# Performance work log

Measured on AMD Instinct MI355X. Metric: run time of the kernel, lower is better.

Reference implementation:

```python
import jax, jax.numpy as jnp
import numpy as np

N = 40000      # nodes
E = 20000      # hyperedges
M = 640000     # incidences
D = 128        # num_features == num_classes == MLP_hidden
ALPHA = 0.1
EPS = 1e-5


def _layernorm(h, g, b):
    mu = jnp.mean(h, axis=-1, keepdims=True)
    var = jnp.mean((h - mu) ** 2, axis=-1, keepdims=True)
    return (h - mu) * jax.lax.rsqrt(var + EPS) * g + b


def _mlp(x, w1, b1, g, be, w2, b2):
    h = x @ w1 + b1
    h = jax.nn.relu(_layernorm(h, g, be))
    return h @ w2 + b2


def _scatter_mean(vals, idx, num_segments):
    s = jax.ops.segment_sum(vals, idx, num_segments=num_segments)
    cnt = jax.ops.segment_sum(jnp.ones((vals.shape[0],), vals.dtype), idx,
                              num_segments=num_segments)
    return s / jnp.maximum(cnt, 1.0)[:, None]


def setup_inputs() -> dict:
    key = jax.random.key(0)
    ks = jax.random.split(key, 16)
    x = jax.random.normal(ks[0], (N, D), dtype=jnp.float32)
    vertex = jax.random.randint(ks[1], (M,), 0, N)
    edges = jax.random.randint(ks[2], (M,), 0, E)
    edge_index = jnp.stack([vertex, edges]).astype(jnp.int64)

    def lin(k, fin, fout):
        s = 1.0 / np.sqrt(fin)
        kw, kb = jax.random.split(k)
        return (jax.random.uniform(kw, (fin, fout), jnp.float32, -s, s),
                jax.random.uniform(kb, (fout,), jnp.float32, -s, s))

    w1_1, b1_1 = lin(ks[3], D, D)
    w1_2, b1_2 = lin(ks[4], D, D)
    w2_1, b2_1 = lin(ks[5], 2 * D, D)
    w2_2, b2_2 = lin(ks[6], D, D)
    g1 = jnp.ones((D,), jnp.float32)
    be1 = jnp.zeros((D,), jnp.float32)
    g2 = jnp.ones((D,), jnp.float32)
    be2 = jnp.zeros((D,), jnp.float32)
    return {"x": x, "w1_1": w1_1, "b1_1": b1_1, "g1": g1, "be1": be1,
            "w1_2": w1_2, "b1_2": b1_2, "w2_1": w2_1, "b2_1": b2_1,
            "g2": g2, "be2": be2, "w2_2": w2_2, "b2_2": b2_2,
            "edge_index": edge_index}


def reference(x, w1_1, b1_1, g1, be1, w1_2, b1_2,
              w2_1, b2_1, g2, be2, w2_2, b2_2, edge_index):
    vertex = edge_index[0]
    edges = edge_index[1]
    X0 = x
    # gather -> MLP1 -> scatter-mean onto hyperedges
    Xve = _mlp(x[vertex], w1_1, b1_1, g1, be1, w1_2, b1_2)   # [M, D]
    Xe = _scatter_mean(Xve, edges, E)                         # [E, D]
    # gather back -> concat -> MLP2 -> scatter-mean onto nodes
    Xev = Xe[edges]                                           # [M, D]
    Xev = _mlp(jnp.concatenate([x[vertex], Xev], axis=-1),
               w2_1, b2_1, g2, be2, w2_2, b2_2)               # [M, D]
    Xv = _scatter_mean(Xev, vertex, N)                        # [N, D]
    return (1.0 - ALPHA) * Xv + ALPHA * X0
```

## Files before the change

kernel.cpp:

```cpp
#include <hip/hip_runtime.h>

#define DF 128
constexpr int NN = 40000;
constexpr int EE = 20000;
constexpr int MM = 640000;
constexpr float EPSF = 1e-5f;
constexpr float ALPHA = 0.1f;
constexpr int SE = 88;
constexpr int SV = 56;

__global__ __launch_bounds__(256) void buildk(const int* __restrict__ ei,
                                              int* __restrict__ cnt_e,
                                              int* __restrict__ cnt_v,
                                              ushort* __restrict__ lst_e,
                                              ushort* __restrict__ lst_v) {
  int m = blockIdx.x * 256 + threadIdx.x;
  int v = ei[m];
  int e = ei[MM + m];
  int pe = atomicAdd(&cnt_e[e], 1);
  lst_e[e * SE + pe] = (ushort)v;
  int pv = atomicAdd(&cnt_v[v], 1);
  lst_v[v * SV + pv] = (ushort)e;
}

__global__ __launch_bounds__(128) void combok(const float* __restrict__ w1_2,
                                              const float* __restrict__ b1_2,
                                              const float* __restrict__ w2_1,
                                              float* __restrict__ Wc,
                                              float* __restrict__ bc) {
  const float* w2b = w2_1 + 128 * DF;
  int j = threadIdx.x;
  if (blockIdx.x < 128) {
    int i = blockIdx.x;
    float s = 0.0f;
    for (int k = 0; k < 128; ++k) s += w1_2[i * DF + k] * w2b[k * DF + j];
    Wc[i * DF + j] = s;
  } else {
    float s = 0.0f;
    for (int k = 0; k < 128; ++k) s += b1_2[k] * w2b[k * DF + j];
    bc[j] = s;
  }
}

__global__ __launch_bounds__(256) void gather1(const float* __restrict__ H1,
                                               const int* __restrict__ cnt_e,
                                               const ushort* __restrict__ lst_e,
                                               float* __restrict__ Hemean) {
  int e = blockIdx.x * 4 + (threadIdx.x >> 6);
  int lane = threadIdx.x & 63;
  int g = lane >> 4;
  int l = lane & 15;
  int deg = cnt_e[e];
  const ushort* lst = lst_e + e * SE;
  float4 acc0 = make_float4(0.f, 0.f, 0.f, 0.f);
  float4 acc1 = make_float4(0.f, 0.f, 0.f, 0.f);
  for (int i = g; i < deg; i += 4) {
    int v = lst[i];
    const float* src = H1 + (size_t)v * DF + l * 8;
    float4 h0 = *reinterpret_cast<const float4*>(src);
    float4 h1 = *reinterpret_cast<const float4*>(src + 4);
    acc0.x += h0.x; acc0.y += h0.y; acc0.z += h0.z; acc0.w += h0.w;
    acc1.x += h1.x; acc1.y += h1.y; acc1.z += h1.z; acc1.w += h1.w;
  }
  #pragma unroll
  for (int mask = 16; mask <= 32; mask <<= 1) {
    acc0.x += __shfl_xor(acc0.x, mask); acc0.y += __shfl_xor(acc0.y, mask);
    acc0.z += __shfl_xor(acc0.z, mask); acc0.w += __shfl_xor(acc0.w, mask);
    acc1.x += __shfl_xor(acc1.x, mask); acc1.y += __shfl_xor(acc1.y, mask);
    acc1.z += __shfl_xor(acc1.z, mask); acc1.w += __shfl_xor(acc1.w, mask);
  }
  if (g == 0) {
    float sc = 1.0f / (float)(deg > 1 ? deg : 1);
    float* dst = Hemean + (size_t)e * DF + l * 8;
    *reinterpret_cast<float4*>(dst) =
        make_float4(acc0.x * sc, acc0.y * sc, acc0.z * sc, acc0.w * sc);
    *reinterpret_cast<float4*>(dst + 4) =
        make_float4(acc1.x * sc, acc1.y * sc, acc1.z * sc, acc1.w * sc);
  }
}

__global__ __launch_bounds__(256) void gather2(const float* __restrict__ A2,
                                               const float* __restrict__ B,
                                               const float* __restrict__ sA,
                                               const float* __restrict__ qA,
                                               const float* __restrict__ sB,
                                               const float* __restrict__ qB,
                                               const int* __restrict__ cnt_v,
                                               const ushort* __restrict__ lst_v,
                                               const float* __restrict__ g2,
                                               const float* __restrict__ be2,
                                               float* __restrict__ Svmean) {
  int v = blockIdx.x * 4 + (threadIdx.x >> 6);
  int lane = threadIdx.x & 63;
  int g = lane >> 4;
  int l = lane & 15;
  const float* ap = A2 + (size_t)v * DF + l * 8;
  float4 a0 = *reinterpret_cast<const float4*>(ap);
  float4 a1 = *reinterpret_cast<const float4*>(ap + 4);
  float4 gv0 = *reinterpret_cast<const float4*>(g2 + l * 8);
  float4 gv1 = *reinterpret_cast<const float4*>(g2 + l * 8 + 4);
  float4 bv0 = *reinterpret_cast<const float4*>(be2 + l * 8);
  float4 bv1 = *reinterpret_cast<const float4*>(be2 + l * 8 + 4);
  float sAv = sA[v];
  float qAv = qA[v];
  int deg = cnt_v[v];
  const ushort* lst = lst_v + v * SV;
  float4 acc0 = make_float4(0.f, 0.f, 0.f, 0.f);
  float4 acc1 = make_float4(0.f, 0.f, 0.f, 0.f);
  for (int i = g; i < deg; i += 4) {
    int e = lst[i];
    const float* bp = B + (size_t)e * DF + l * 8;
    float4 b0 = *reinterpret_cast<const float4*>(bp);
    float4 b1 = *reinterpret_cast<const float4*>(bp + 4);
    float d = a0.x * b0.x + a0.y * b0.y + a0.z * b0.z + a0.w * b0.w +
              a1.x * b1.x + a1.y * b1.y + a1.z * b1.z + a1.w * b1.w;
    d += __shfl_xor(d, 1, 16);
    d += __shfl_xor(d, 2, 16);
    d += __shfl_xor(d, 4, 16);
    d += __shfl_xor(d, 8, 16);
    float s = sAv + sB[e];
    float q = qAv + qB[e] + 2.0f * d;
    float mean = s * (1.0f / 128.0f);
    float var = q * (1.0f / 128.0f) - mean * mean;
    float rs = rsqrtf(var + EPSF);
    float mrs = mean * rs;
    float t;
    t = (a0.x + b0.x) * rs - mrs; acc0.x += fmaxf(t * gv0.x + bv0.x, 0.f);
    t = (a0.y + b0.y) * rs - mrs; acc0.y += fmaxf(t * gv0.y + bv0.y, 0.f);
    t = (a0.z + b0.z) * rs - mrs; acc0.z += fmaxf(t * gv0.z + bv0.z, 0.f);
    t = (a0.w + b0.w) * rs - mrs; acc0.w += fmaxf(t * gv0.w + bv0.w, 0.f);
    t = (a1.x + b1.x) * rs - mrs; acc1.x += fmaxf(t * gv1.x + bv1.x, 0.f);
    t = (a1.y + b1.y) * rs - mrs; acc1.y += fmaxf(t * gv1.y + bv1.y, 0.f);
    t = (a1.z + b1.z) * rs - mrs; acc1.z += fmaxf(t * gv1.z + bv1.z, 0.f);
    t = (a1.w + b1.w) * rs - mrs; acc1.w += fmaxf(t * gv1.w + bv1.w, 0.f);
  }
  #pragma unroll
  for (int mask = 16; mask <= 32; mask <<= 1) {
    acc0.x += __shfl_xor(acc0.x, mask); acc0.y += __shfl_xor(acc0.y, mask);
    acc0.z += __shfl_xor(acc0.z, mask); acc0.w += __shfl_xor(acc0.w, mask);
    acc1.x += __shfl_xor(acc1.x, mask); acc1.y += __shfl_xor(acc1.y, mask);
    acc1.z += __shfl_xor(acc1.z, mask); acc1.w += __shfl_xor(acc1.w, mask);
  }
  if (g == 0) {
    float sc = 1.0f / (float)(deg > 1 ? deg : 1);
    float* dst = Svmean + (size_t)v * DF + l * 8;
    *reinterpret_cast<float4*>(dst) =
        make_float4(acc0.x * sc, acc0.y * sc, acc0.z * sc, acc0.w * sc);
    *reinterpret_cast<float4*>(dst + 4) =
        make_float4(acc1.x * sc, acc1.y * sc, acc1.z * sc, acc1.w * sc);
  }
}

template <int EPI, bool STATS>
__global__ __launch_bounds__(256) void gemm128(const float* __restrict__ A, int nrows,
                                               const float* __restrict__ W,
                                               const float* __restrict__ bias,
                                               const float* __restrict__ bias2,
                                               const int* __restrict__ cnt,
                                               const float* __restrict__ g,
                                               const float* __restrict__ be,
                                               const float* __restrict__ xres,
                                               float* __restrict__ C,
                                               float* __restrict__ sOut,
                                               float* __restrict__ qOut) {
  __shared__ float as[64 * 132];
  int tid = threadIdx.x;
  int rbase = blockIdx.x * 64;

  #pragma unroll
  for (int j = 0; j < 8; ++j) {
    int q = tid + j * 256;
    int row = q >> 5;
    int c4 = q & 31;
    int grow = rbase + row;
    float4 v = make_float4(0.f, 0.f, 0.f, 0.f);
    if (grow < nrows) {
      v = *reinterpret_cast<const float4*>(A + (size_t)grow * DF + c4 * 4);
    }
    *reinterpret_cast<float4*>(&as[row * 132 + c4 * 4]) = v;
  }
  __syncthreads();

  int tc = tid & 15;
  int tr = tid >> 4;
  int cbase = tc * 8;

  float acc[4][8];
  #pragma unroll
  for (int i = 0; i < 4; ++i)
    #pragma unroll
    for (int c = 0; c < 8; ++c) acc[i][c] = 0.0f;

  #pragma unroll 4
  for (int k = 0; k < 128; ++k) {
    float w[8];
    *reinterpret_cast<float4*>(&w[0]) = *reinterpret_cast<const float4*>(W + k * DF + cbase);
    *reinterpret_cast<float4*>(&w[4]) = *reinterpret_cast<const float4*>(W + k * DF + cbase + 4);
    float a[4];
    #pragma unroll
    for (int i = 0; i < 4; ++i) a[i] = as[(tr * 4 + i) * 132 + k];
    #pragma unroll
    for (int i = 0; i < 4; ++i)
      #pragma unroll
      for (int c = 0; c < 8; ++c) acc[i][c] += a[i] * w[c];
  }

  float bv[8];
  #pragma unroll
  for (int c = 0; c < 8; ++c) bv[c] = 0.0f;
  if (bias) {
    #pragma unroll
    for (int c = 0; c < 8; ++c) bv[c] = bias[cbase + c];
  }
  if (bias2) {
    #pragma unroll
    for (int c = 0; c < 8; ++c) bv[c] += bias2[cbase + c];
  }
  #pragma unroll
  for (int i = 0; i < 4; ++i)
    #pragma unroll
    for (int c = 0; c < 8; ++c) acc[i][c] += bv[c];

  if (STATS) {
    #pragma unroll
    for (int i = 0; i < 4; ++i) {
      float s = 0.f, q = 0.f;
      #pragma unroll
      for (int c = 0; c < 8; ++c) { s += acc[i][c]; q += acc[i][c] * acc[i][c]; }
      #pragma unroll
      for (int mask = 1; mask <= 8; mask <<= 1) {
        s += __shfl_xor(s, mask, 16);
        q += __shfl_xor(q, mask, 16);
      }
      if (tc == 0) {
        int grow = rbase + tr * 4 + i;
        if (grow < nrows) { sOut[grow] = s; qOut[grow] = q; }
      }
    }
  }

  if (EPI == 1) {
    float gv[8], bev[8];
    #pragma unroll
    for (int c = 0; c < 8; ++c) { gv[c] = g[cbase + c]; bev[c] = be[cbase + c]; }
    #pragma unroll
    for (int i = 0; i < 4; ++i) {
      float s = 0.f, s2 = 0.f;
      #pragma unroll
      for (int c = 0; c < 8; ++c) { s += acc[i][c]; s2 += acc[i][c] * acc[i][c]; }
      #pragma unroll
      for (int mask = 1; mask <= 8; mask <<= 1) {
        s += __shfl_xor(s, mask, 16);
        s2 += __shfl_xor(s2, mask, 16);
      }
      float mean = s * (1.0f / 128.0f);
      float var = s2 * (1.0f / 128.0f) - mean * mean;
      float rs = rsqrtf(var + EPSF);
      #pragma unroll
      for (int c = 0; c < 8; ++c) {
        float y = (acc[i][c] - mean) * rs * gv[c] + bev[c];
        acc[i][c] = fmaxf(y, 0.0f);
      }
    }
  }

  #pragma unroll
  for (int i = 0; i < 4; ++i) {
    int grow = rbase + tr * 4 + i;
    if (grow >= nrows) continue;
    float outv[8];
    if (EPI == 2) {
      int cv = cnt[grow];
      #pragma unroll
      for (int c = 0; c < 8; ++c) {
        float xv = xres[(size_t)grow * DF + cbase + c];
        outv[c] = (cv == 0) ? ALPHA * xv : (1.0f - ALPHA) * acc[i][c] + ALPHA * xv;
      }
    } else {
      #pragma unroll
      for (int c = 0; c < 8; ++c) outv[c] = acc[i][c];
    }
    *reinterpret_cast<float4*>(C + (size_t)grow * DF + cbase) =
        make_float4(outv[0], outv[1], outv[2], outv[3]);
    *reinterpret_cast<float4*>(C + (size_t)grow * DF + cbase + 4) =
        make_float4(outv[4], outv[5], outv[6], outv[7]);
  }
}

extern "C" void kernel_launch(void* const* d_in, const int* in_sizes, int n_in,
                              void* d_out, int out_size, void* d_ws, size_t ws_size,
                              hipStream_t stream) {
  const float* x    = (const float*)d_in[0];
  const float* w1_1 = (const float*)d_in[1];
  const float* b1_1 = (const float*)d_in[2];
  const float* g1   = (const float*)d_in[3];
  const float* be1  = (const float*)d_in[4];
  const float* w1_2 = (const float*)d_in[5];
  const float* b1_2 = (const float*)d_in[6];
  const float* w2_1 = (const float*)d_in[7];
  const float* b2_1 = (const float*)d_in[8];
  const float* g2   = (const float*)d_in[9];
  const float* be2  = (const float*)d_in[10];
  const float* w2_2 = (const float*)d_in[11];
  const float* b2_2 = (const float*)d_in[12];
  const int* ei     = (const int*)d_in[13];
  float* out = (float*)d_out;

  float* ws = (float*)d_ws;
  float* bufN1 = ws;
  float* bufN2 = ws + 5120000;
  float* bufE  = ws + 10240000;
  float* Wc    = ws + 12800000;
  float* bc    = ws + 12816384;
  float* sA    = ws + 12816512;
  float* qA    = ws + 12856512;
  float* sB    = ws + 12896512;
  float* qB    = ws + 12916512;
  int*   ints  = (int*)(ws + 12936512);
  int* cnt_e  = ints;
  int* cnt_v  = ints + 20000;
  ushort* lst_e = (ushort*)(ints + 60000);
  ushort* lst_v = (ushort*)(ints + 60000 + 880000);

  hipMemsetAsync(cnt_e, 0, 60000 * sizeof(int), stream);

  buildk<<<MM / 256, 256, 0, stream>>>(ei, cnt_e, cnt_v, lst_e, lst_v);

  gemm128<1, false><<<(NN + 63) / 64, 256, 0, stream>>>(
      x, NN, w1_1, b1_1, nullptr, nullptr, g1, be1, nullptr, bufN1,
      nullptr, nullptr);

  combok<<<129, 128, 0, stream>>>(w1_2, b1_2, w2_1, Wc, bc);

  gather1<<<EE / 4, 256, 0, stream>>>(bufN1, cnt_e, lst_e, bufE);

  gemm128<0, true><<<(EE + 63) / 64, 256, 0, stream>>>(
      bufE, EE, Wc, bc, b2_1, nullptr, nullptr, nullptr, nullptr, bufE,
      sB, qB);

  gemm128<0, true><<<(NN + 63) / 64, 256, 0, stream>>>(
      x, NN, w2_1, nullptr, nullptr, nullptr, nullptr, nullptr, nullptr, bufN1,
      sA, qA);

  gather2<<<NN / 4, 256, 0, stream>>>(bufN1, bufE, sA, qA, sB, qB,
                                      cnt_v, lst_v, g2, be2, bufN2);

  gemm128<2, false><<<(NN + 63) / 64, 256, 0, stream>>>(
      bufN2, NN, w2_2, b2_2, nullptr, cnt_v, nullptr, nullptr, x, out,
      nullptr, nullptr);
}
```

Baseline: 398.3 us.

## Merge independent build, node GEMMs and weight-combine into one launch

The incidence-list build, the first-layer node GEMM with LayerNorm, the x@W2a node GEMM with row stats, and the W1_2·W2b combine are now one kernel that picks its role from the block index. The node GEMM is moved ahead of gather1 and the buffers are reassigned so its output survives until gather2. This removes three launch boundaries and lets the atomic-heavy build overlap with the GEMM tiles. In exchange every block of the merged kernel reserves the 33 KB shared tile, including the build blocks that never use it, which may reduce how many build blocks run at once.

```diff
diff --git a/kernel.cpp b/kernel.cpp
--- a/kernel.cpp
+++ b/kernel.cpp
@@ -9,37 +9,207 @@
 constexpr int SE = 88;
 constexpr int SV = 56;
 
-__global__ __launch_bounds__(256) void buildk(const int* __restrict__ ei,
-                                              int* __restrict__ cnt_e,
-                                              int* __restrict__ cnt_v,
-                                              ushort* __restrict__ lst_e,
-                                              ushort* __restrict__ lst_v) {
-  int m = blockIdx.x * 256 + threadIdx.x;
-  int v = ei[m];
-  int e = ei[MM + m];
-  int pe = atomicAdd(&cnt_e[e], 1);
-  lst_e[e * SE + pe] = (ushort)v;
-  int pv = atomicAdd(&cnt_v[v], 1);
-  lst_v[v * SV + pv] = (ushort)e;
-}
-
-__global__ __launch_bounds__(128) void combok(const float* __restrict__ w1_2,
-                                              const float* __restrict__ b1_2,
-                                              const float* __restrict__ w2_1,
-                                              float* __restrict__ Wc,
-                                              float* __restrict__ bc) {
-  const float* w2b = w2_1 + 128 * DF;
-  int j = threadIdx.x;
-  if (blockIdx.x < 128) {
-    int i = blockIdx.x;
-    float s = 0.0f;
-    for (int k = 0; k < 128; ++k) s += w1_2[i * DF + k] * w2b[k * DF + j];
-    Wc[i * DF + j] = s;
+constexpr int NB_BUILD = MM / 256;
+constexpr int NB_GEMM  = (NN + 63) / 64;
+constexpr int NB_COMBO = (128 * 128 + 128 + 255) / 256;
+
+template <int EPI, bool STATS>
+__device__ __forceinline__ void gemm_tile(const float* __restrict__ A, int nrows,
+                                          const float* __restrict__ W,
+                                          const float* __restrict__ bias,
+                                          const float* __restrict__ bias2,
+                                          const int* __restrict__ cnt,
+                                          const float* __restrict__ g,
+                                          const float* __restrict__ be,
+                                          const float* __restrict__ xres,
+                                          float* __restrict__ C,
+                                          float* __restrict__ sOut,
+                                          float* __restrict__ qOut,
+                                          int blk, float* as) {
+  int tid = threadIdx.x;
+  int rbase = blk * 64;
+
+  #pragma unroll
+  for (int j = 0; j < 8; ++j) {
+    int q = tid + j * 256;
+    int row = q >> 5;
+    int c4 = q & 31;
+    int grow = rbase + row;
+    float4 v = make_float4(0.f, 0.f, 0.f, 0.f);
+    if (grow < nrows) {
+      v = *reinterpret_cast<const float4*>(A + (size_t)grow * DF + c4 * 4);
+    }
+    *reinterpret_cast<float4*>(&as[row * 132 + c4 * 4]) = v;
+  }
+  __syncthreads();
+
+  int tc = tid & 15;
+  int tr = tid >> 4;
+  int cbase = tc * 8;
+
+  float acc[4][8];
+  #pragma unroll
+  for (int i = 0; i < 4; ++i)
+    #pragma unroll
+    for (int c = 0; c < 8; ++c) acc[i][c] = 0.0f;
+
+  #pragma unroll 4
+  for (int k = 0; k < 128; ++k) {
+    float w[8];
+    *reinterpret_cast<float4*>(&w[0]) = *reinterpret_cast<const float4*>(W + k * DF + cbase);
+    *reinterpret_cast<float4*>(&w[4]) = *reinterpret_cast<const float4*>(W + k * DF + cbase + 4);
+    float a[4];
+    #pragma unroll
+    for (int i = 0; i < 4; ++i) a[i] = as[(tr * 4 + i) * 132 + k];
+    #pragma unroll
+    for (int i = 0; i < 4; ++i)
+      #pragma unroll
+      for (int c = 0; c < 8; ++c) acc[i][c] += a[i] * w[c];
+  }
+
+  float bv[8];
+  #pragma unroll
+  for (int c = 0; c < 8; ++c) bv[c] = 0.0f;
+  if (bias) {
+    #pragma unroll
+    for (int c = 0; c < 8; ++c) bv[c] = bias[cbase + c];
+  }
+  if (bias2) {
+    #pragma unroll
+    for (int c = 0; c < 8; ++c) bv[c] += bias2[cbase + c];
+  }
+  #pragma unroll
+  for (int i = 0; i < 4; ++i)
+    #pragma unroll
+    for (int c = 0; c < 8; ++c) acc[i][c] += bv[c];
+
+  if (STATS) {
+    #pragma unroll
+    for (int i = 0; i < 4; ++i) {
+      float s = 0.f, q = 0.f;
+      #pragma unroll
+      for (int c = 0; c < 8; ++c) { s += acc[i][c]; q += acc[i][c] * acc[i][c]; }
+      #pragma unroll
+      for (int mask = 1; mask <= 8; mask <<= 1) {
+        s += __shfl_xor(s, mask, 16);
+        q += __shfl_xor(q, mask, 16);
+      }
+      if (tc == 0) {
+        int grow = rbase + tr * 4 + i;
+        if (grow < nrows) { sOut[grow] = s; qOut[grow] = q; }
+      }
+    }
+  }
+
+  if (EPI == 1) {
+    float gv[8], bev[8];
+    #pragma unroll
+    for (int c = 0; c < 8; ++c) { gv[c] = g[cbase + c]; bev[c] = be[cbase + c]; }
+    #pragma unroll
+    for (int i = 0; i < 4; ++i) {
+      float s = 0.f, s2 = 0.f;
+      #pragma unroll
+      for (int c = 0; c < 8; ++c) { s += acc[i][c]; s2 += acc[i][c] * acc[i][c]; }
+      #pragma unroll
+      for (int mask = 1; mask <= 8; mask <<= 1) {
+        s += __shfl_xor(s, mask, 16);
+        s2 += __shfl_xor(s2, mask, 16);
+      }
+      float mean = s * (1.0f / 128.0f);
+      float var = s2 * (1.0f / 128.0f) - mean * mean;
+      float rs = rsqrtf(var + EPSF);
+      #pragma unroll
+      for (int c = 0; c < 8; ++c) {
+        float y = (acc[i][c] - mean) * rs * gv[c] + bev[c];
+        acc[i][c] = fmaxf(y, 0.0f);
+      }
+    }
+  }
+
+  #pragma unroll
+  for (int i = 0; i < 4; ++i) {
+    int grow = rbase + tr * 4 + i;
+    if (grow >= nrows) continue;
+    float outv[8];
+    if (EPI == 2) {
+      int cv = cnt[grow];
+      #pragma unroll
+      for (int c = 0; c < 8; ++c) {
+        float xv = xres[(size_t)grow * DF + cbase + c];
+        outv[c] = (cv == 0) ? ALPHA * xv : (1.0f - ALPHA) * acc[i][c] + ALPHA * xv;
+      }
+    } else {
+      #pragma unroll
+      for (int c = 0; c < 8; ++c) outv[c] = acc[i][c];
+    }
+    *reinterpret_cast<float4*>(C + (size_t)grow * DF + cbase) =
+        make_float4(outv[0], outv[1], outv[2], outv[3]);
+    *reinterpret_cast<float4*>(C + (size_t)grow * DF + cbase + 4) =
+        make_float4(outv[4], outv[5], outv[6], outv[7]);
+  }
+}
+
+__global__ __launch_bounds__(256) void fusedA(
+    const int* __restrict__ ei,
+    int* __restrict__ cnt_e, int* __restrict__ cnt_v,
+    ushort* __restrict__ lst_e, ushort* __restrict__ lst_v,
+    const float* __restrict__ x,
+    const float* __restrict__ w1_1, const float* __restrict__ b1_1,
+    const float* __restrict__ g1, const float* __restrict__ be1,
+    const float* __restrict__ w2_1,
+    const float* __restrict__ w1_2, const float* __restrict__ b1_2,
+    float* __restrict__ H1, float* __restrict__ A2,
+    float* __restrict__ sA, float* __restrict__ qA,
+    float* __restrict__ Wc, float* __restrict__ bc) {
+  __shared__ float as[64 * 132];
+  int blk = blockIdx.x;
+  if (blk < NB_BUILD) {
+    int m = blk * 256 + threadIdx.x;
+    int v = ei[m];
+    int e = ei[MM + m];
+    int pe = atomicAdd(&cnt_e[e], 1);
+    lst_e[e * SE + pe] = (ushort)v;
+    int pv = atomicAdd(&cnt_v[v], 1);
+    lst_v[v * SV + pv] = (ushort)e;
+  } else if (blk < NB_BUILD + NB_GEMM) {
+    gemm_tile<1, false>(x, NN, w1_1, b1_1, nullptr, nullptr, g1, be1, nullptr,
+                        H1, nullptr, nullptr, blk - NB_BUILD, as);
+  } else if (blk < NB_BUILD + 2 * NB_GEMM) {
+    gemm_tile<0, true>(x, NN, w2_1, nullptr, nullptr, nullptr, nullptr, nullptr,
+                       nullptr, A2, sA, qA, blk - NB_BUILD - NB_GEMM, as);
   } else {
-    float s = 0.0f;
-    for (int k = 0; k < 128; ++k) s += b1_2[k] * w2b[k * DF + j];
-    bc[j] = s;
-  }
+    const float* w2b = w2_1 + 128 * DF;
+    int out = (blk - NB_BUILD - 2 * NB_GEMM) * 256 + threadIdx.x;
+    if (out < 16384) {
+      int i = out >> 7;
+      int j = out & 127;
+      float s = 0.0f;
+      for (int k = 0; k < 128; ++k) s += w1_2[i * DF + k] * w2b[k * DF + j];
+      Wc[out] = s;
+    } else if (out < 16512) {
+      int j = out - 16384;
+      float s = 0.0f;
+      for (int k = 0; k < 128; ++k) s += b1_2[k] * w2b[k * DF + j];
+      bc[j] = s;
+    }
+  }
+}
+
+template <int EPI, bool STATS>
+__global__ __launch_bounds__(256) void gemm128(const float* __restrict__ A, int nrows,
+                                               const float* __restrict__ W,
+                                               const float* __restrict__ bias,
+                                               const float* __restrict__ bias2,
+                                               const int* __restrict__ cnt,
+                                               const float* __restrict__ g,
+                                               const float* __restrict__ be,
+                                               const float* __restrict__ xres,
+                                               float* __restrict__ C,
+                                               float* __restrict__ sOut,
+                                               float* __restrict__ qOut) {
+  __shared__ float as[64 * 132];
+  gemm_tile<EPI, STATS>(A, nrows, W, bias, bias2, cnt, g, be, xres, C, sOut,
+                        qOut, blockIdx.x, as);
 }
 
 __global__ __launch_bounds__(256) void gather1(const float* __restrict__ H1,
@@ -151,142 +321,6 @@
   }
 }
 
-template <int EPI, bool STATS>
-__global__ __launch_bounds__(256) void gemm128(const float* __restrict__ A, int nrows,
-                                               const float* __restrict__ W,
-                                               const float* __restrict__ bias,
-                                               const float* __restrict__ bias2,
-                                               const int* __restrict__ cnt,
-                                               const float* __restrict__ g,
-                                               const float* __restrict__ be,
-                                               const float* __restrict__ xres,
-                                               float* __restrict__ C,
-                                               float* __restrict__ sOut,
-                                               float* __restrict__ qOut) {
-  __shared__ float as[64 * 132];
-  int tid = threadIdx.x;
-  int rbase = blockIdx.x * 64;
-
-  #pragma unroll
-  for (int j = 0; j < 8; ++j) {
-    int q = tid + j * 256;
-    int row = q >> 5;
-    int c4 = q & 31;
-    int grow = rbase + row;
-    float4 v = make_float4(0.f, 0.f, 0.f, 0.f);
-    if (grow < nrows) {
-      v = *reinterpret_cast<const float4*>(A + (size_t)grow * DF + c4 * 4);
-    }
-    *reinterpret_cast<float4*>(&as[row * 132 + c4 * 4]) = v;
-  }
-  __syncthreads();
-
-  int tc = tid & 15;
-  int tr = tid >> 4;
-  int cbase = tc * 8;
-
-  float acc[4][8];
-  #pragma unroll
-  for (int i = 0; i < 4; ++i)
-    #pragma unroll
-    for (int c = 0; c < 8; ++c) acc[i][c] = 0.0f;
-
-  #pragma unroll 4
-  for (int k = 0; k < 128; ++k) {
-    float w[8];
-    *reinterpret_cast<float4*>(&w[0]) = *reinterpret_cast<const float4*>(W + k * DF + cbase);
-    *reinterpret_cast<float4*>(&w[4]) = *reinterpret_cast<const float4*>(W + k * DF + cbase + 4);
-    float a[4];
-    #pragma unroll
-    for (int i = 0; i < 4; ++i) a[i] = as[(tr * 4 + i) * 132 + k];
-    #pragma unroll
-    for (int i = 0; i < 4; ++i)
-      #pragma unroll
-      for (int c = 0; c < 8; ++c) acc[i][c] += a[i] * w[c];
-  }
-
-  float bv[8];
-  #pragma unroll
-  for (int c = 0; c < 8; ++c) bv[c] = 0.0f;
-  if (bias) {
-    #pragma unroll
-    for (int c = 0; c < 8; ++c) bv[c] = bias[cbase + c];
-  }
-  if (bias2) {
-    #pragma unroll
-    for (int c = 0; c < 8; ++c) bv[c] += bias2[cbase + c];
-  }
-  #pragma unroll
-  for (int i = 0; i < 4; ++i)
-    #pragma unroll
-    for (int c = 0; c < 8; ++c) acc[i][c] += bv[c];
-
-  if (STATS) {
-    #pragma unroll
-    for (int i = 0; i < 4; ++i) {
-      float s = 0.f, q = 0.f;
-      #pragma unroll
-      for (int c = 0; c < 8; ++c) { s += acc[i][c]; q += acc[i][c] * acc[i][c]; }
-      #pragma unroll
-      for (int mask = 1; mask <= 8; mask <<= 1) {
-        s += __shfl_xor(s, mask, 16);
-        q += __shfl_xor(q, mask, 16);
-      }
-      if (tc == 0) {
-        int grow = rbase + tr * 4 + i;
-        if (grow < nrows) { sOut[grow] = s; qOut[grow] = q; }
-      }
-    }
-  }
-
-  if (EPI == 1) {
-    float gv[8], bev[8];
-    #pragma unroll
-    for (int c = 0; c < 8; ++c) { gv[c] = g[cbase + c]; bev[c] = be[cbase + c]; }
-    #pragma unroll
-    for (int i = 0; i < 4; ++i) {
-      float s = 0.f, s2 = 0.f;
-      #pragma unroll
-      for (int c = 0; c < 8; ++c) { s += acc[i][c]; s2 += acc[i][c] * acc[i][c]; }
-      #pragma unroll
-      for (int mask = 1; mask <= 8; mask <<= 1) {
-        s += __shfl_xor(s, mask, 16);
-        s2 += __shfl_xor(s2, mask, 16);
-      }
-      float mean = s * (1.0f / 128.0f);
-      float var = s2 * (1.0f / 128.0f) - mean * mean;
-      float rs = rsqrtf(var + EPSF);
-      #pragma unroll
-      for (int c = 0; c < 8; ++c) {
-        float y = (acc[i][c] - mean) * rs * gv[c] + bev[c];
-        acc[i][c] = fmaxf(y, 0.0f);
-      }
-    }
-  }
-
-  #pragma unroll
-  for (int i = 0; i < 4; ++i) {
-    int grow = rbase + tr * 4 + i;
-    if (grow >= nrows) continue;
-    float outv[8];
-    if (EPI == 2) {
-      int cv = cnt[grow];
-      #pragma unroll
-      for (int c = 0; c < 8; ++c) {
-        float xv = xres[(size_t)grow * DF + cbase + c];
-        outv[c] = (cv == 0) ? ALPHA * xv : (1.0f - ALPHA) * acc[i][c] + ALPHA * xv;
-      }
-    } else {
-      #pragma unroll
-      for (int c = 0; c < 8; ++c) outv[c] = acc[i][c];
-    }
-    *reinterpret_cast<float4*>(C + (size_t)grow * DF + cbase) =
-        make_float4(outv[0], outv[1], outv[2], outv[3]);
-    *reinterpret_cast<float4*>(C + (size_t)grow * DF + cbase + 4) =
-        make_float4(outv[4], outv[5], outv[6], outv[7]);
-  }
-}
-
 extern "C" void kernel_launch(void* const* d_in, const int* in_sizes, int n_in,
                               void* d_out, int out_size, void* d_ws, size_t ws_size,
                               hipStream_t stream) {
@@ -324,28 +358,19 @@
 
   hipMemsetAsync(cnt_e, 0, 60000 * sizeof(int), stream);
 
-  buildk<<<MM / 256, 256, 0, stream>>>(ei, cnt_e, cnt_v, lst_e, lst_v);
-
-  gemm128<1, false><<<(NN + 63) / 64, 256, 0, stream>>>(
-      x, NN, w1_1, b1_1, nullptr, nullptr, g1, be1, nullptr, bufN1,
+  fusedA<<<NB_BUILD + 2 * NB_GEMM + NB_COMBO, 256, 0, stream>>>(
+      ei, cnt_e, cnt_v, lst_e, lst_v, x, w1_1, b1_1, g1, be1, w2_1, w1_2, b1_2,
+      bufN1, bufN2, sA, qA, Wc, bc);
+
+  gather1<<<EE / 4, 256, 0, stream>>>(bufN1, cnt_e, lst_e, bufE);
+
+  gemm128<0, true><<<(EE + 63) / 64, 256, 0, stream>>>(
+      bufE, EE, Wc, bc, b2_1, nullptr, nullptr, nullptr, nullptr, bufE, sB, qB);
+
+  gather2<<<NN / 4, 256, 0, stream>>>(bufN2, bufE, sA, qA, sB, qB,
+                                      cnt_v, lst_v, g2, be2, bufN1);
+
+  gemm128<2, false><<<(NN + 63) / 64, 256, 0, stream>>>(
+      bufN1, NN, w2_2, b2_2, nullptr, cnt_v, nullptr, nullptr, x, out,
       nullptr, nullptr);
-
-  combok<<<129, 128, 0, stream>>>(w1_2, b1_2, w2_1, Wc, bc);
-
-  gather1<<<EE / 4, 256, 0, stream>>>(bufN1, cnt_e, lst_e, bufE);
-
-  gemm128<0, true><<<(EE + 63) / 64, 256, 0, stream>>>(
-      bufE, EE, Wc, bc, b2_1, nullptr, nullptr, nullptr, nullptr, bufE,
-      sB, qB);
-
-  gemm128<0, true><<<(NN + 63) / 64, 256, 0, stream>>>(
-      x, NN, w2_1, nullptr, nullptr, nullptr, nullptr, nullptr, nullptr, bufN1,
-      sA, qA);
-
-  gather2<<<NN / 4, 256, 0, stream>>>(bufN1, bufE, sA, qA, sB, qB,
-                                      cnt_v, lst_v, g2, be2, bufN2);
-
-  gemm128<2, false><<<(NN + 63) / 64, 256, 0, stream>>>(
-      bufN2, NN, w2_2, b2_2, nullptr, cnt_v, nullptr, nullptr, x, out,
-      nullptr, nullptr);
-}
+}
```

New measurement: 387.1 us. 1.03x faster.
